# Kernel tuning notes

Hardware: AMD Instinct MI355X
Metric: run time of the kernel (lower is better)

The kernel has to match this reference:

```python
import jax, jax.numpy as jnp
import numpy as np

ALPHA = 0.25
GAMMA = 2
IGNORE_INDEX = 255
LOSS_WEIGHT = 1.0
NUM_CLASSES = 19


def setup_inputs() -> dict:
    key = jax.random.key(0)
    k1, k2 = jax.random.split(key)
    N, C, H, W = 4, NUM_CLASSES, 512, 512
    cls_score = jax.random.normal(k1, (N, C, H, W), dtype=jnp.float32)
    label = jax.random.randint(k2, (N, H, W), 0, NUM_CLASSES, dtype=jnp.int64)
    return {"cls_score": cls_score, "label": label}


def reference(cls_score, label):
    # _expand_onehot_labels: valid pixels get a one-hot channel vector
    valid = (label >= 0) & (label != IGNORE_INDEX)          # [N,H,W]
    safe_lab = jnp.where(valid, label, 0)
    onehot = jax.nn.one_hot(safe_lab, cls_score.shape[1], axis=1,
                            dtype=cls_score.dtype)          # [N,C,H,W]
    validf = valid.astype(cls_score.dtype)[:, None, :, :]   # [N,1,H,W]
    onehot = onehot * validf

    # Focal class weight. NOTE: the original torch code uses the RAW logits
    # (temp_pred = pred.cpu()), not sigmoid(pred), when computing the weight.
    x = cls_score
    class_weight = jnp.where(onehot == 1,
                             ALPHA * (1.0 - x) ** GAMMA,
                             ALPHA * x ** GAMMA)            # [N,C,H,W]

    # binary_cross_entropy_with_logits, reduction='none', weight=class_weight
    bce = jnp.maximum(x, 0) - x * onehot + jnp.log1p(jnp.exp(-jnp.abs(x)))
    loss = bce * class_weight

    # weight_reduce_loss with weight=valid_mask (expanded), reduction='mean'
    loss = (loss * validf).mean()
    return LOSS_WEIGHT * loss
```

## Files before the change

### kernel.cpp

```cpp
#include <hip/hip_runtime.h>


#define NC 19
#define IGNORE_INDEX 255
#define ALPHA 0.25f

typedef float f32x4 __attribute__((ext_vector_type(4)));
typedef int   i32x4 __attribute__((ext_vector_type(4)));

constexpr int NBATCH = 4;
constexpr int HW = 512 * 512;
constexpr int NQ = NBATCH * NC * (HW / 4);
constexpr int BLOCK = 256;
constexpr int QPT = 4;
constexpr int GRID = NQ / (BLOCK * QPT);
constexpr int TT = GRID * BLOCK;
constexpr int BLOCK2 = 1024;
constexpr float INV_TOTAL = 1.0f / (float)(NBATCH * NC * HW);

constexpr float A0 =  0.0485865f;
constexpr float A1 = -0.1402039f;
constexpr float A2 =  0.2024491f;
constexpr float A3 = -0.2005852f;
constexpr float A4 =  0.1182934f;
constexpr float A5 = -0.0048016f;
constexpr float A6 = -0.0214538f;

template <int NWAVE>
__device__ __forceinline__ float block_reduce(float v, float* smem) {
    #pragma unroll
    for (int off = 32; off > 0; off >>= 1)
        v += __shfl_down(v, off, 64);
    const int lane = threadIdx.x & 63;
    const int wid  = threadIdx.x >> 6;
    if (lane == 0) smem[wid] = v;
    __syncthreads();
    float s = 0.0f;
    if (threadIdx.x == 0) {
        #pragma unroll
        for (int i = 0; i < NWAVE; ++i) s += smem[i];
    }
    return s;
}

__device__ __forceinline__ float quad_loss(const f32x4 v, const i32x4 l4,
                                           const int c) {
    float acc = 0.0f;
    #pragma unroll
    for (int j = 0; j < 4; ++j) {
        const float xv  = v[j];
        const int   lb  = l4[j];
        const bool  val = (lb >= 0) && (lb != IGNORE_INDEX);
        const bool  t   = (lb == c);

        const float u  = fminf(fabsf(xv), 6.0f);
        const float xx = fmaf(u, 0.33333333f, -1.0f);
        float sp = A6;
        sp = fmaf(sp, xx, A5);
        sp = fmaf(sp, xx, A4);
        sp = fmaf(sp, xx, A3);
        sp = fmaf(sp, xx, A2);
        sp = fmaf(sp, xx, A1);
        sp = fmaf(sp, xx, A0);

        const float y   = t ? -xv : xv;
        const float d   = y + (t ? 1.0f : 0.0f);
        const float w   = (val ? ALPHA : 0.0f) * d * d;
        const float bce = fmaxf(y, 0.0f) + sp;
        acc = fmaf(bce, w, acc);
    }
    return acc;
}

__global__ __launch_bounds__(BLOCK, 8) void focal_partial(
        const f32x4* __restrict__ x,
        const i32x4* __restrict__ lab4,
        float*       __restrict__ partial) {
    const int tid = blockIdx.x * BLOCK + threadIdx.x;

    int c_[QPT];
    int li_[QPT];
    #pragma unroll
    for (int k = 0; k < QPT; ++k) {
        const int      q     = tid + k * TT;
        const unsigned plane = (unsigned)q >> 16;
        const unsigned n     = plane / NC;
        c_[k]  = (int)(plane - n * NC);
        li_[k] = (int)((n << 16) + (q & 65535));
    }

    f32x4 v0 = x[tid + 0 * TT], v1 = x[tid + 1 * TT],
          v2 = x[tid + 2 * TT], v3 = x[tid + 3 * TT];
    i32x4 l0 = lab4[li_[0]], l1 = lab4[li_[1]],
          l2 = lab4[li_[2]], l3 = lab4[li_[3]];
    asm volatile("" : "+v"(v0), "+v"(v1), "+v"(v2), "+v"(v3),
                      "+v"(l0), "+v"(l1), "+v"(l2), "+v"(l3));

    float acc = quad_loss(v0, l0, c_[0]);
    acc += quad_loss(v1, l1, c_[1]);
    acc += quad_loss(v2, l2, c_[2]);
    acc += quad_loss(v3, l3, c_[3]);

    __shared__ float smem[BLOCK / 64];
    const float s = block_reduce<BLOCK / 64>(acc, smem);
    if (threadIdx.x == 0) partial[blockIdx.x] = s;
}

__global__ __launch_bounds__(BLOCK2) void focal_finalize(
        const float* __restrict__ partial,
        float*       __restrict__ out) {
    float acc = 0.0f;
    for (int i = threadIdx.x; i < GRID; i += BLOCK2)
        acc += partial[i];
    __shared__ float smem[BLOCK2 / 64];
    const float s = block_reduce<BLOCK2 / 64>(acc, smem);
    if (threadIdx.x == 0) out[0] = s * INV_TOTAL;
}

extern "C" void kernel_launch(void* const* d_in, const int* in_sizes, int n_in,
                              void* d_out, int out_size, void* d_ws, size_t ws_size,
                              hipStream_t stream) {
    const f32x4* cls_score = (const f32x4*)d_in[0];
    const i32x4* lab4      = (const i32x4*)d_in[1];
    float* out     = (float*)d_out;
    float* partial = (float*)d_ws;

    focal_partial<<<GRID, BLOCK, 0, stream>>>(cls_score, lab4, partial);
    focal_finalize<<<1, BLOCK2, 0, stream>>>(partial, out);
}
```

Baseline: 21.20 us.

## Loop over all classes per pixel quad so labels load once

Each thread now owns one quad of four pixels and walks all 19 class planes for it. The label vector is loaded once per thread and the validity weight is computed once, instead of reloading labels for every class plane. This removes redundant label traffic and the per-element division that recovered plane indices. The grid shrinks to a quarter of its former block count, and each thread issues 19 strided loads, so latency hiding now relies on more in-flight loads per thread rather than on more threads.

```diff
diff --git a/kernel.cpp b/kernel.cpp
--- a/kernel.cpp
+++ b/kernel.cpp
@@ -10,11 +10,10 @@
 
 constexpr int NBATCH = 4;
 constexpr int HW = 512 * 512;
-constexpr int NQ = NBATCH * NC * (HW / 4);
+constexpr int QPP = HW / 4;
+constexpr int NP = NBATCH * QPP;
 constexpr int BLOCK = 256;
-constexpr int QPT = 4;
-constexpr int GRID = NQ / (BLOCK * QPT);
-constexpr int TT = GRID * BLOCK;
+constexpr int GRID = NP / BLOCK;
 constexpr int BLOCK2 = 1024;
 constexpr float INV_TOTAL = 1.0f / (float)(NBATCH * NC * HW);
 
@@ -43,63 +42,51 @@
     return s;
 }
 
-__device__ __forceinline__ float quad_loss(const f32x4 v, const i32x4 l4,
-                                           const int c) {
-    float acc = 0.0f;
-    #pragma unroll
-    for (int j = 0; j < 4; ++j) {
-        const float xv  = v[j];
-        const int   lb  = l4[j];
-        const bool  val = (lb >= 0) && (lb != IGNORE_INDEX);
-        const bool  t   = (lb == c);
-
-        const float u  = fminf(fabsf(xv), 6.0f);
-        const float xx = fmaf(u, 0.33333333f, -1.0f);
-        float sp = A6;
-        sp = fmaf(sp, xx, A5);
-        sp = fmaf(sp, xx, A4);
-        sp = fmaf(sp, xx, A3);
-        sp = fmaf(sp, xx, A2);
-        sp = fmaf(sp, xx, A1);
-        sp = fmaf(sp, xx, A0);
-
-        const float y   = t ? -xv : xv;
-        const float d   = y + (t ? 1.0f : 0.0f);
-        const float w   = (val ? ALPHA : 0.0f) * d * d;
-        const float bce = fmaxf(y, 0.0f) + sp;
-        acc = fmaf(bce, w, acc);
-    }
-    return acc;
-}
-
-__global__ __launch_bounds__(BLOCK, 8) void focal_partial(
+__global__ __launch_bounds__(BLOCK) void focal_partial(
         const f32x4* __restrict__ x,
         const i32x4* __restrict__ lab4,
         float*       __restrict__ partial) {
-    const int tid = blockIdx.x * BLOCK + threadIdx.x;
+    const int p  = blockIdx.x * BLOCK + threadIdx.x;
+    const int n  = p >> 16;
+    const int pq = p & (QPP - 1);
 
-    int c_[QPT];
-    int li_[QPT];
+    const i32x4 l4 = lab4[p];
+    int   lab[4];
+    float av[4];
     #pragma unroll
-    for (int k = 0; k < QPT; ++k) {
-        const int      q     = tid + k * TT;
-        const unsigned plane = (unsigned)q >> 16;
-        const unsigned n     = plane / NC;
-        c_[k]  = (int)(plane - n * NC);
-        li_[k] = (int)((n << 16) + (q & 65535));
+    for (int j = 0; j < 4; ++j) {
+        lab[j] = l4[j];
+        av[j]  = ((lab[j] >= 0) && (lab[j] != IGNORE_INDEX)) ? ALPHA : 0.0f;
     }
 
-    f32x4 v0 = x[tid + 0 * TT], v1 = x[tid + 1 * TT],
-          v2 = x[tid + 2 * TT], v3 = x[tid + 3 * TT];
-    i32x4 l0 = lab4[li_[0]], l1 = lab4[li_[1]],
-          l2 = lab4[li_[2]], l3 = lab4[li_[3]];
-    asm volatile("" : "+v"(v0), "+v"(v1), "+v"(v2), "+v"(v3),
-                      "+v"(l0), "+v"(l1), "+v"(l2), "+v"(l3));
+    const f32x4* base = x + ((size_t)(n * NC) << 16) + pq;
 
-    float acc = quad_loss(v0, l0, c_[0]);
-    acc += quad_loss(v1, l1, c_[1]);
-    acc += quad_loss(v2, l2, c_[2]);
-    acc += quad_loss(v3, l3, c_[3]);
+    float acc = 0.0f;
+    #pragma unroll
+    for (int c = 0; c < NC; ++c) {
+        const f32x4 v = base[(size_t)c << 16];
+        #pragma unroll
+        for (int j = 0; j < 4; ++j) {
+            const float xv = v[j];
+            const bool  t  = (lab[j] == c);
+
+            const float u  = fminf(fabsf(xv), 6.0f);
+            const float xx = fmaf(u, 0.33333333f, -1.0f);
+            float sp = A6;
+            sp = fmaf(sp, xx, A5);
+            sp = fmaf(sp, xx, A4);
+            sp = fmaf(sp, xx, A3);
+            sp = fmaf(sp, xx, A2);
+            sp = fmaf(sp, xx, A1);
+            sp = fmaf(sp, xx, A0);
+
+            const float y   = t ? -xv : xv;
+            const float d   = y + (t ? 1.0f : 0.0f);
+            const float w   = av[j] * d * d;
+            const float bce = fmaxf(y, 0.0f) + sp;
+            acc = fmaf(bce, w, acc);
+        }
+    }
 
     __shared__ float smem[BLOCK / 64];
     const float s = block_reduce<BLOCK / 64>(acc, smem);
```

Measured after the change: 20.69 us. -2.4%, faster.
